# Kernel tuning notes

Measured on AMD Instinct MI355X. Metric: run time of the kernel, lower is better.

## Reference

```python
import jax, jax.numpy as jnp
import numpy as np

D_MODEL = 1024
N_HEADS = 16
DEPTH = D_MODEL // N_HEADS
B, S = 2, 2048


def layer_norm(x, gamma, beta):
    # Faithful to the torch module: unbiased std (ddof=1), eps added to std.
    mean = jnp.mean(x, axis=-1, keepdims=True)
    std = jnp.std(x, axis=-1, ddof=1, keepdims=True)
    return gamma * ((x - mean) / (std + 1e-6)) + beta


def setup_inputs() -> dict:
    key = jax.random.key(0)
    ks = jax.random.split(key, 12)
    sc = 0.02
    x = jax.random.normal(ks[0], (B, S, D_MODEL), jnp.float32)
    mask = jnp.triu(jnp.ones((S, S), jnp.float32), k=1)  # 1 where masked (future)
    return {
        "x": x,
        "mask": mask,
        "wq_w": jax.random.normal(ks[1], (D_MODEL, D_MODEL), jnp.float32) * sc,
        "wq_b": jnp.zeros((D_MODEL,), jnp.float32),
        "wk_w": jax.random.normal(ks[2], (D_MODEL, D_MODEL), jnp.float32) * sc,
        "wk_b": jnp.zeros((D_MODEL,), jnp.float32),
        "wv_w": jax.random.normal(ks[3], (D_MODEL, D_MODEL), jnp.float32) * sc,
        "wv_b": jnp.zeros((D_MODEL,), jnp.float32),
        "dense_w": jax.random.normal(ks[4], (D_MODEL, D_MODEL), jnp.float32) * sc,
        "dense_b": jnp.zeros((D_MODEL,), jnp.float32),
        "gamma1": jnp.ones((D_MODEL,), jnp.float32),
        "beta1": jnp.zeros((D_MODEL,), jnp.float32),
        "gamma2": jnp.ones((D_MODEL,), jnp.float32),
        "beta2": jnp.zeros((D_MODEL,), jnp.float32),
        "fc_w": jax.random.normal(ks[5], (4 * D_MODEL, D_MODEL), jnp.float32) * sc,
        "proj_w": jax.random.normal(ks[6], (D_MODEL, 4 * D_MODEL), jnp.float32) * sc,
    }


def reference(x, mask, wq_w, wq_b, wk_w, wk_b, wv_w, wv_b, dense_w, dense_b,
              gamma1, beta1, gamma2, beta2, fc_w, proj_w):
    # x: [B,S,D]. Dropout is identity in eval.
    xn = layer_norm(x, gamma1, beta1)

    def split(h):  # [B,S,D] -> [B,H,S,depth]
        return h.reshape(B, S, N_HEADS, DEPTH).transpose(0, 2, 1, 3)

    q = split(xn @ wq_w.T + wq_b)
    k = split(xn @ wk_w.T + wk_b)
    v = split(xn @ wv_w.T + wv_b)

    scores = jnp.einsum("bhqd,bhkd->bhqk", q, k) / jnp.sqrt(
        jnp.asarray(DEPTH, jnp.float32))
    scores = scores + mask * -1e9
    attn = jax.nn.softmax(scores, axis=-1)
    ctx = jnp.einsum("bhqk,bhkd->bhqd", attn, v)
    ctx = ctx.transpose(0, 2, 1, 3).reshape(B, S, D_MODEL)
    attn_out = ctx @ dense_w.T + dense_b

    # Residual adds the *normed* x (faithful to the original ordering).
    h = xn + attn_out
    hn = layer_norm(h, gamma2, beta2)

    ff = jax.nn.gelu(hn @ fc_w.T, approximate=False) @ proj_w.T
    return hn + ff
```

## Files before the change

kernel.cpp:

```cpp
#include <hip/hip_runtime.h>
#include <math.h>

typedef __bf16 bf16;
typedef __attribute__((ext_vector_type(2))) __bf16 bf16x2;
typedef __attribute__((ext_vector_type(4))) __bf16 bf16x4;
typedef __attribute__((ext_vector_type(8))) __bf16 bf16x8;
typedef __attribute__((ext_vector_type(4))) float f32x4;

#define D_MODEL 1024
#define NH 16
#define DP 64
#define BB 2
#define SEQ 2048
#define TOK 4096
#define FFD 4096
#define AST 72

__device__ __forceinline__ void async16(bf16* lds, const bf16* g) {
    __builtin_amdgcn_global_load_lds(
        (__attribute__((address_space(1))) void*)g,
        (__attribute__((address_space(3))) void*)lds, 16, 0, 0);
}

__device__ __forceinline__ f32x4 mfma16(bf16x8 a, bf16x8 b, f32x4 c) {
    return __builtin_amdgcn_mfma_f32_16x16x32_bf16(a, b, c, 0, 0, 0);
}

struct CvtArgs {
    const float4* in[6];
    bf16x4* out[6];
};
__global__ __launch_bounds__(256) void cvt_all(CvtArgs a)
{
    const int i = blockIdx.x * 256 + threadIdx.x;
    int seg, idx;
    if (i < (1 << 20)) { seg = i >> 18; idx = i & ((1 << 18) - 1); }
    else {
        const int j = i - (1 << 20);
        seg = 4 + (j >> 20); idx = j & ((1 << 20) - 1);
    }
    const float4 v = a.in[seg][idx];
    bf16x4 o; o[0] = (bf16)v.x; o[1] = (bf16)v.y; o[2] = (bf16)v.z; o[3] = (bf16)v.w;
    a.out[seg][idx] = o;
}

template<typename TIN>
__global__ __launch_bounds__(256) void ln_kernel(
    const TIN* __restrict__ in, const float* __restrict__ g,
    const float* __restrict__ be, bf16* __restrict__ out)
{
    const size_t row = blockIdx.x;
    const int t = threadIdx.x;
    const TIN* x = in + row * D_MODEL;

    float v0, v1, v2, v3;
    if constexpr (sizeof(TIN) == 4) {
        const float4 xv = *(const float4*)(x + t * 4);
        v0 = xv.x; v1 = xv.y; v2 = xv.z; v3 = xv.w;
    } else {
        const bf16x4 xv = *(const bf16x4*)(x + t * 4);
        v0 = (float)xv[0]; v1 = (float)xv[1]; v2 = (float)xv[2]; v3 = (float)xv[3];
    }
    float s  = v0 + v1 + v2 + v3;
    float ss = v0*v0 + v1*v1 + v2*v2 + v3*v3;
    #pragma unroll
    for (int off = 32; off > 0; off >>= 1) {
        s  += __shfl_down(s, off);
        ss += __shfl_down(ss, off);
    }
    __shared__ float rs[4], rss[4];
    if ((t & 63) == 0) { rs[t >> 6] = s; rss[t >> 6] = ss; }
    __syncthreads();
    const float S  = rs[0] + rs[1] + rs[2] + rs[3];
    const float SS = rss[0] + rss[1] + rss[2] + rss[3];
    const float mean = S * (1.0f / 1024.0f);
    const float var  = fmaxf((SS - S * mean) * (1.0f / 1023.0f), 0.0f);
    const float inv  = 1.0f / (sqrtf(var) + 1e-6f);

    const float4 gv = *(const float4*)(g  + t * 4);
    const float4 bv = *(const float4*)(be + t * 4);
    bf16x4 ov;
    ov[0] = (bf16)(gv.x * ((v0 - mean) * inv) + bv.x);
    ov[1] = (bf16)(gv.y * ((v1 - mean) * inv) + bv.y);
    ov[2] = (bf16)(gv.z * ((v2 - mean) * inv) + bv.z);
    ov[3] = (bf16)(gv.w * ((v3 - mean) * inv) + bv.w);
    *(bf16x4*)(out + row * D_MODEL + t * 4) = ov;
}

template<int EPI, typename TOUT>
__global__ __launch_bounds__(256, 2) void gemm_bt(
    const bf16* __restrict__ A, const bf16* __restrict__ W,
    const float* __restrict__ bias, const bf16* res,
    TOUT* C, int M, int N, int K, float scale)
{
    __shared__ __align__(16) bf16 As[128 * 32];
    __shared__ __align__(16) bf16 Bs[128 * 32];
    const int t = threadIdx.x;
    const int w = t >> 6, lane = t & 63;
    const int fr = lane & 15, quad = lane >> 4;
    const int m0 = blockIdx.y * 128, n0 = blockIdx.x * 128;
    const int wm = (w >> 1) * 64, wn = (w & 1) * 64;

    const f32x4 z = {0.f, 0.f, 0.f, 0.f};
    f32x4 acc[4][4];
    #pragma unroll
    for (int i = 0; i < 4; ++i)
        #pragma unroll
        for (int j = 0; j < 4; ++j) acc[i][j] = z;

    const int nk = K >> 5;
    for (int kt = 0; kt < nk; ++kt) {
        const int k0 = kt << 5;
        #pragma unroll
        for (int call = 0; call < 2; ++call) {
            const int c = call * 256 + t;
            const int row = c >> 2, sub = c & 3;
            async16(&As[(size_t)(call * 256 + w * 64) * 8],
                    A + (size_t)(m0 + row) * K + k0 + sub * 8);
            async16(&Bs[(size_t)(call * 256 + w * 64) * 8],
                    W + (size_t)(n0 + row) * K + k0 + sub * 8);
        }
        __syncthreads();
        bf16x8 af[4], bfr[4];
        #pragma unroll
        for (int i = 0; i < 4; ++i)
            af[i] = *(const bf16x8*)&As[(wm + i * 16 + fr) * 32 + quad * 8];
        #pragma unroll
        for (int j = 0; j < 4; ++j)
            bfr[j] = *(const bf16x8*)&Bs[(wn + j * 16 + fr) * 32 + quad * 8];
        #pragma unroll
        for (int i = 0; i < 4; ++i)
            #pragma unroll
            for (int j = 0; j < 4; ++j)
                acc[i][j] = mfma16(af[i], bfr[j], acc[i][j]);
        __syncthreads();
    }

    #pragma unroll
    for (int i = 0; i < 4; ++i) {
        #pragma unroll
        for (int j = 0; j < 4; ++j) {
            #pragma unroll
            for (int r = 0; r < 4; ++r) {
                const int m = m0 + wm + i * 16 + quad * 4 + r;
                const int n = n0 + wn + j * 16 + fr;
                float v = acc[i][j][r];
                if (EPI == 1) {
                    v += bias[n];
                    v += (float)res[(size_t)m * N + n];
                    C[(size_t)m * N + n] = (TOUT)v;
                } else if (EPI == 2) {
                    v = 0.5f * v * (1.0f + erff(v * 0.70710678118f));
                    C[(size_t)m * N + n] = (TOUT)v;
                } else {
                    v += (float)res[(size_t)m * N + n];
                    C[(size_t)m * N + n] = (TOUT)v;
                }
            }
        }
    }
}

template<int EPI, typename TOUT>
__global__ __launch_bounds__(256, 2) void gemm_bt64(
    const bf16* __restrict__ A, const bf16* __restrict__ W,
    const float* __restrict__ bias, const bf16* res,
    TOUT* C, int M, int N, int K)
{
    __shared__ __align__(16) bf16 As[128 * 32];
    __shared__ __align__(16) bf16 Bs[64 * 32];
    const int t = threadIdx.x;
    const int w = t >> 6, lane = t & 63;
    const int fr = lane & 15, quad = lane >> 4;
    const int m0 = blockIdx.y * 128, n0 = blockIdx.x * 64;
    const int wm = (w >> 1) * 64, wn = (w & 1) * 32;

    const f32x4 z = {0.f, 0.f, 0.f, 0.f};
    f32x4 acc[4][2];
    #pragma unroll
    for (int i = 0; i < 4; ++i)
        #pragma unroll
        for (int j = 0; j < 2; ++j) acc[i][j] = z;

    const int nk = K >> 5;
    for (int kt = 0; kt < nk; ++kt) {
        const int k0 = kt << 5;
        #pragma unroll
        for (int call = 0; call < 2; ++call) {
            const int c = call * 256 + t;
            const int row = c >> 2, sub = c & 3;
            async16(&As[(size_t)(call * 256 + w * 64) * 8],
                    A + (size_t)(m0 + row) * K + k0 + sub * 8);
        }
        {
            const int row = t >> 2, sub = t & 3;
            async16(&Bs[(size_t)(w * 64) * 8],
                    W + (size_t)(n0 + row) * K + k0 + sub * 8);
        }
        __syncthreads();
        bf16x8 af[4], bfr[2];
        #pragma unroll
        for (int i = 0; i < 4; ++i)
            af[i] = *(const bf16x8*)&As[(wm + i * 16 + fr) * 32 + quad * 8];
        #pragma unroll
        for (int j = 0; j < 2; ++j)
            bfr[j] = *(const bf16x8*)&Bs[(wn + j * 16 + fr) * 32 + quad * 8];
        #pragma unroll
        for (int i = 0; i < 4; ++i)
            #pragma unroll
            for (int j = 0; j < 2; ++j)
                acc[i][j] = mfma16(af[i], bfr[j], acc[i][j]);
        __syncthreads();
    }

    #pragma unroll
    for (int i = 0; i < 4; ++i) {
        #pragma unroll
        for (int j = 0; j < 2; ++j) {
            #pragma unroll
            for (int r = 0; r < 4; ++r) {
                const int m = m0 + wm + i * 16 + quad * 4 + r;
                const int n = n0 + wn + j * 16 + fr;
                float v = acc[i][j][r];
                if (EPI == 1) {
                    v += bias[n];
                    v += (float)res[(size_t)m * N + n];
                    C[(size_t)m * N + n] = (TOUT)v;
                } else {
                    v += (float)res[(size_t)m * N + n];
                    C[(size_t)m * N + n] = (TOUT)v;
                }
            }
        }
    }
}

__global__ __launch_bounds__(256, 2) void gemm_qkv(
    const bf16* __restrict__ A,
    const bf16* __restrict__ wq, const bf16* __restrict__ wk,
    const bf16* __restrict__ wvv,
    const float* __restrict__ bq, const float* __restrict__ bk,
    const float* __restrict__ bv,
    bf16* __restrict__ outq, bf16* __restrict__ outk, bf16* __restrict__ outv)
{
    const int sel = blockIdx.x >> 3;
    const bf16* W = (sel == 0) ? wq : ((sel == 1) ? wk : wvv);
    const float* bias = (sel == 0) ? bq : ((sel == 1) ? bk : bv);
    bf16* C = (sel == 0) ? outq : ((sel == 1) ? outk : outv);
    const float scale = (sel == 0) ? 0.125f : 1.0f;
    const int K = D_MODEL;

    __shared__ __align__(16) bf16 As[128 * 32];
    __shared__ __align__(16) bf16 Bs[128 * 32];
    const int t = threadIdx.x;
    const int w = t >> 6, lane = t & 63;
    const int fr = lane & 15, quad = lane >> 4;
    const int m0 = blockIdx.y * 128, n0 = (blockIdx.x & 7) * 128;
    const int wm = (w >> 1) * 64, wn = (w & 1) * 64;

    const f32x4 z = {0.f, 0.f, 0.f, 0.f};
    f32x4 acc[4][4];
    #pragma unroll
    for (int i = 0; i < 4; ++i)
        #pragma unroll
        for (int j = 0; j < 4; ++j) acc[i][j] = z;

    for (int kt = 0; kt < (D_MODEL >> 5); ++kt) {
        const int k0 = kt << 5;
        #pragma unroll
        for (int call = 0; call < 2; ++call) {
            const int c = call * 256 + t;
            const int row = c >> 2, sub = c & 3;
            async16(&As[(size_t)(call * 256 + w * 64) * 8],
                    A + (size_t)(m0 + row) * K + k0 + sub * 8);
            async16(&Bs[(size_t)(call * 256 + w * 64) * 8],
                    W + (size_t)(n0 + row) * K + k0 + sub * 8);
        }
        __syncthreads();
        bf16x8 af[4], bfr[4];
        #pragma unroll
        for (int i = 0; i < 4; ++i)
            af[i] = *(const bf16x8*)&As[(wm + i * 16 + fr) * 32 + quad * 8];
        #pragma unroll
        for (int j = 0; j < 4; ++j)
            bfr[j] = *(const bf16x8*)&Bs[(wn + j * 16 + fr) * 32 + quad * 8];
        #pragma unroll
        for (int i = 0; i < 4; ++i)
            #pragma unroll
            for (int j = 0; j < 4; ++j)
                acc[i][j] = mfma16(af[i], bfr[j], acc[i][j]);
        __syncthreads();
    }

    #pragma unroll
    for (int i = 0; i < 4; ++i)
        #pragma unroll
        for (int j = 0; j < 4; ++j)
            #pragma unroll
            for (int r = 0; r < 4; ++r) {
                const int m = m0 + wm + i * 16 + quad * 4 + r;
                const int n = n0 + wn + j * 16 + fr;
                const float vv = (acc[i][j][r] + bias[n]) * scale;
                const int b = m >> 11, s = m & 2047, h = n >> 6, d = n & 63;
                C[(((size_t)(b * NH + h)) * SEQ + s) * DP + d] = (bf16)vv;
            }
}

__global__ __launch_bounds__(256, 2) void attn_kernel(
    const bf16* __restrict__ q, const bf16* __restrict__ k,
    const bf16* __restrict__ v, bf16* __restrict__ ctx)
{
    __shared__ __align__(16) bf16 Ks[2][64 * AST];
    __shared__ __align__(16) bf16 VsT[2][64 * AST];
    __shared__ __align__(16) bf16 Ps[4][16 * AST];
    const int t = threadIdx.x, wv = t >> 6, lane = t & 63;
    const int fr = lane & 15, quad = lane >> 4;
    const int bh = blockIdx.y;
    const size_t base = (size_t)bh * SEQ * DP;
    const int b = bh >> 4, hh = bh & 15;
    const f32x4 z = {0.f, 0.f, 0.f, 0.f};
    const int krow = t >> 2, kd0 = (t & 3) * 16;
    const int pp = t & 31, c0 = (t >> 5) * 8;

    for (int half = 0; half < 2; ++half) {
        const int qt = half ? (31 - (int)blockIdx.x) : (int)blockIdx.x;
        const int q0 = qt * 64, qr0 = q0 + wv * 16;
        const int nkt = qt + 1;

        __syncthreads();

        bf16x8 qf[2];
        #pragma unroll
        for (int c = 0; c < 2; ++c)
            qf[c] = *(const bf16x8*)(q + base + (size_t)(qr0 + fr) * DP + c * 32 + quad * 8);

        bf16x8 k0r, k1r, v0r, v1r;
        {
            const bf16* kp = k + base + (size_t)krow * DP + kd0;
            k0r = *(const bf16x8*)kp; k1r = *(const bf16x8*)(kp + 8);
            const bf16* vp = v + base + (size_t)(2 * pp) * DP + c0;
            v0r = *(const bf16x8*)vp; v1r = *(const bf16x8*)(vp + DP);
        }

        f32x4 o[4] = {z, z, z, z};
        float mi[4] = {-1e30f, -1e30f, -1e30f, -1e30f};
        float li[4] = {0.f, 0.f, 0.f, 0.f};

        for (int kt = 0; kt < nkt; ++kt) {
            const int cur = kt & 1;
            const int kk0 = kt * 64;
            *(bf16x8*)&Ks[cur][krow * AST + kd0]     = k0r;
            *(bf16x8*)&Ks[cur][krow * AST + kd0 + 8] = k1r;
            #pragma unroll
            for (int j = 0; j < 8; ++j) {
                bf16x2 pr; pr[0] = v0r[j]; pr[1] = v1r[j];
                *(bf16x2*)&VsT[cur][(c0 + j) * AST + 2 * pp] = pr;
            }
            __syncthreads();
            if (kt + 1 < nkt) {
                const bf16* kp = k + base + (size_t)(kk0 + 64 + krow) * DP + kd0;
                k0r = *(const bf16x8*)kp; k1r = *(const bf16x8*)(kp + 8);
                const bf16* vp = v + base + (size_t)(kk0 + 64 + 2 * pp) * DP + c0;
                v0r = *(const bf16x8*)vp; v1r = *(const bf16x8*)(vp + DP);
            }

            f32x4 sa[4] = {z, z, z, z};
            #pragma unroll
            for (int nb = 0; nb < 4; ++nb)
                #pragma unroll
                for (int c = 0; c < 2; ++c) {
                    const bf16x8 kf = *(const bf16x8*)&Ks[cur][(nb * 16 + fr) * AST + c * 32 + quad * 8];
                    sa[nb] = mfma16(qf[c], kf, sa[nb]);
                }

            float p[4][4], rmax[4];
            #pragma unroll
            for (int r = 0; r < 4; ++r) rmax[r] = -1e30f;
            #pragma unroll
            for (int nb = 0; nb < 4; ++nb)
                #pragma unroll
                for (int r = 0; r < 4; ++r) {
                    const int key = kk0 + nb * 16 + fr;
                    const int qrow = qr0 + quad * 4 + r;
                    float sv = sa[nb][r];
                    if (key > qrow) sv += -1e9f;
                    p[nb][r] = sv;
                    rmax[r] = fmaxf(rmax[r], sv);
                }
            #pragma unroll
            for (int off = 1; off < 16; off <<= 1)
                #pragma unroll
                for (int r = 0; r < 4; ++r)
                    rmax[r] = fmaxf(rmax[r], __shfl_xor(rmax[r], off));

            float alpha[4], psum[4];
            #pragma unroll
            for (int r = 0; r < 4; ++r) {
                const float nm = fmaxf(mi[r], rmax[r]);
                alpha[r] = __expf(mi[r] - nm);
                mi[r] = nm;
                float ps = 0.f;
                #pragma unroll
                for (int nb = 0; nb < 4; ++nb) {
                    const float e = __expf(p[nb][r] - nm);
                    p[nb][r] = e;
                    ps += e;
                }
                psum[r] = ps;
            }
            #pragma unroll
            for (int off = 1; off < 16; off <<= 1)
                #pragma unroll
                for (int r = 0; r < 4; ++r)
                    psum[r] += __shfl_xor(psum[r], off);
            #pragma unroll
            for (int r = 0; r < 4; ++r) li[r] = li[r] * alpha[r] + psum[r];
            #pragma unroll
            for (int db = 0; db < 4; ++db)
                #pragma unroll
                for (int r = 0; r < 4; ++r) o[db][r] *= alpha[r];

            #pragma unroll
            for (int nb = 0; nb < 4; ++nb)
                #pragma unroll
                for (int r = 0; r < 4; ++r)
                    Ps[wv][(quad * 4 + r) * AST + nb * 16 + fr] = (bf16)p[nb][r];

            bf16x8 pf[2];
            #pragma unroll
            for (int c = 0; c < 2; ++c)
                pf[c] = *(const bf16x8*)&Ps[wv][fr * AST + c * 32 + quad * 8];
            #pragma unroll
            for (int db = 0; db < 4; ++db)
                #pragma unroll
                for (int c = 0; c < 2; ++c) {
                    const bf16x8 vf = *(const bf16x8*)&VsT[cur][(db * 16 + fr) * AST + c * 32 + quad * 8];
                    o[db] = mfma16(pf[c], vf, o[db]);
                }
        }

        #pragma unroll
        for (int db = 0; db < 4; ++db)
            #pragma unroll
            for (int r = 0; r < 4; ++r) {
                const int qrow = qr0 + quad * 4 + r;
                const int d = db * 16 + fr;
                ctx[((size_t)(b * SEQ + qrow)) * D_MODEL + hh * DP + d] =
                    (bf16)(o[db][r] / li[r]);
            }
    }
}

extern "C" void kernel_launch(void* const* d_in, const int* in_sizes, int n_in,
                              void* d_out, int out_size, void* d_ws, size_t ws_size,
                              hipStream_t stream) {
    const float* x       = (const float*)d_in[0];
    const float* wq_w    = (const float*)d_in[2];
    const float* wq_b    = (const float*)d_in[3];
    const float* wk_w    = (const float*)d_in[4];
    const float* wk_b    = (const float*)d_in[5];
    const float* wv_w    = (const float*)d_in[6];
    const float* wv_b    = (const float*)d_in[7];
    const float* dense_w = (const float*)d_in[8];
    const float* dense_b = (const float*)d_in[9];
    const float* gamma1  = (const float*)d_in[10];
    const float* beta1   = (const float*)d_in[11];
    const float* gamma2  = (const float*)d_in[12];
    const float* beta2   = (const float*)d_in[13];
    const float* fc_w    = (const float*)d_in[14];
    const float* proj_w  = (const float*)d_in[15];
    float* out = (float*)d_out;

    bf16* ws = (bf16*)d_ws;
    const size_t M1 = (size_t)1 << 20;
    bf16* xn   = ws;
    bf16* qb   = ws + 4 * M1;
    bf16* kb   = ws + 8 * M1;
    bf16* vb   = ws + 12 * M1;
    bf16* ctx  = ws + 16 * M1;
    bf16* ff1  = qb;
    bf16* wqc  = ws + 20 * M1;
    bf16* wkc  = ws + 21 * M1;
    bf16* wvc  = ws + 22 * M1;
    bf16* wdc  = ws + 23 * M1;
    bf16* fcc  = ws + 24 * M1;
    bf16* prjc = ws + 28 * M1;
    bf16* h = xn, *hn = xn;

    CvtArgs ca;
    ca.in[0] = (const float4*)wq_w;    ca.out[0] = (bf16x4*)wqc;
    ca.in[1] = (const float4*)wk_w;    ca.out[1] = (bf16x4*)wkc;
    ca.in[2] = (const float4*)wv_w;    ca.out[2] = (bf16x4*)wvc;
    ca.in[3] = (const float4*)dense_w; ca.out[3] = (bf16x4*)wdc;
    ca.in[4] = (const float4*)fc_w;    ca.out[4] = (bf16x4*)fcc;
    ca.in[5] = (const float4*)proj_w;  ca.out[5] = (bf16x4*)prjc;
    cvt_all<<<12288, 256, 0, stream>>>(ca);

    ln_kernel<float><<<TOK, 256, 0, stream>>>(x, gamma1, beta1, xn);
    gemm_qkv<<<dim3(24, 32), 256, 0, stream>>>(xn, wqc, wkc, wvc,
                                               wq_b, wk_b, wv_b, qb, kb, vb);
    attn_kernel<<<dim3(16, BB * NH), 256, 0, stream>>>(qb, kb, vb, ctx);
    gemm_bt64<1, bf16><<<dim3(16, 32), 256, 0, stream>>>(ctx, wdc, dense_b, xn, h,
                                                         TOK, D_MODEL, D_MODEL);
    ln_kernel<bf16><<<TOK, 256, 0, stream>>>(h, gamma2, beta2, hn);
    gemm_bt<2, bf16><<<dim3(32, 32), 256, 0, stream>>>(hn, fcc, nullptr, nullptr, ff1,
                                                       TOK, FFD, D_MODEL, 1.0f);
    gemm_bt64<3, float><<<dim3(16, 32), 256, 0, stream>>>(ff1, prjc, nullptr, hn, out,
                                                          TOK, D_MODEL, FFD);
}
```

Measured before the change: 404.6 us.

## Double-buffer LDS tiles in GEMM kernels to prefetch next K-slice

The three GEMM kernels (gemm_bt, gemm_bt64, gemm_qkv) now use two LDS buffers for each operand. The first K-tile is loaded before the loop, and each iteration issues async loads for the next tile while running MFMAs on the current one. This hides global-to-LDS load latency behind compute and drops one barrier per iteration. In exchange, LDS use per block doubles, and overlap only happens if the end-of-loop barrier's memory wait falls after the MFMAs.

```diff
diff --git a/kernel.cpp b/kernel.cpp
--- a/kernel.cpp
+++ b/kernel.cpp
@@ -93,8 +93,8 @@
     const float* __restrict__ bias, const bf16* res,
     TOUT* C, int M, int N, int K, float scale)
 {
-    __shared__ __align__(16) bf16 As[128 * 32];
-    __shared__ __align__(16) bf16 Bs[128 * 32];
+    __shared__ __align__(16) bf16 As[2][128 * 32];
+    __shared__ __align__(16) bf16 Bs[2][128 * 32];
     const int t = threadIdx.x;
     const int w = t >> 6, lane = t & 63;
     const int fr = lane & 15, quad = lane >> 4;
@@ -109,25 +109,38 @@
         for (int j = 0; j < 4; ++j) acc[i][j] = z;
 
     const int nk = K >> 5;
+    const int srow = t >> 2, ssub = t & 3;
+
+    #pragma unroll
+    for (int call = 0; call < 2; ++call) {
+        const int row = call * 64 + srow;
+        async16(&As[0][(size_t)(call * 256 + w * 64) * 8],
+                A + (size_t)(m0 + row) * K + ssub * 8);
+        async16(&Bs[0][(size_t)(call * 256 + w * 64) * 8],
+                W + (size_t)(n0 + row) * K + ssub * 8);
+    }
+    __syncthreads();
+
     for (int kt = 0; kt < nk; ++kt) {
-        const int k0 = kt << 5;
-        #pragma unroll
-        for (int call = 0; call < 2; ++call) {
-            const int c = call * 256 + t;
-            const int row = c >> 2, sub = c & 3;
-            async16(&As[(size_t)(call * 256 + w * 64) * 8],
-                    A + (size_t)(m0 + row) * K + k0 + sub * 8);
-            async16(&Bs[(size_t)(call * 256 + w * 64) * 8],
-                    W + (size_t)(n0 + row) * K + k0 + sub * 8);
-        }
-        __syncthreads();
+        const int cur = kt & 1;
+        if (kt + 1 < nk) {
+            const int k0 = (kt + 1) << 5;
+            #pragma unroll
+            for (int call = 0; call < 2; ++call) {
+                const int row = call * 64 + srow;
+                async16(&As[cur ^ 1][(size_t)(call * 256 + w * 64) * 8],
+                        A + (size_t)(m0 + row) * K + k0 + ssub * 8);
+                async16(&Bs[cur ^ 1][(size_t)(call * 256 + w * 64) * 8],
+                        W + (size_t)(n0 + row) * K + k0 + ssub * 8);
+            }
+        }
         bf16x8 af[4], bfr[4];
         #pragma unroll
         for (int i = 0; i < 4; ++i)
-            af[i] = *(const bf16x8*)&As[(wm + i * 16 + fr) * 32 + quad * 8];
+            af[i] = *(const bf16x8*)&As[cur][(wm + i * 16 + fr) * 32 + quad * 8];
         #pragma unroll
         for (int j = 0; j < 4; ++j)
-            bfr[j] = *(const bf16x8*)&Bs[(wn + j * 16 + fr) * 32 + quad * 8];
+            bfr[j] = *(const bf16x8*)&Bs[cur][(wn + j * 16 + fr) * 32 + quad * 8];
         #pragma unroll
         for (int i = 0; i < 4; ++i)
             #pragma unroll
@@ -167,8 +180,8 @@
     const float* __restrict__ bias, const bf16* res,
     TOUT* C, int M, int N, int K)
 {
-    __shared__ __align__(16) bf16 As[128 * 32];
-    __shared__ __align__(16) bf16 Bs[64 * 32];
+    __shared__ __align__(16) bf16 As[2][128 * 32];
+    __shared__ __align__(16) bf16 Bs[2][64 * 32];
     const int t = threadIdx.x;
     const int w = t >> 6, lane = t & 63;
     const int fr = lane & 15, quad = lane >> 4;
@@ -183,28 +196,38 @@
         for (int j = 0; j < 2; ++j) acc[i][j] = z;
 
     const int nk = K >> 5;
+    const int srow = t >> 2, ssub = t & 3;
+
+    #pragma unroll
+    for (int call = 0; call < 2; ++call) {
+        const int row = call * 64 + srow;
+        async16(&As[0][(size_t)(call * 256 + w * 64) * 8],
+                A + (size_t)(m0 + row) * K + ssub * 8);
+    }
+    async16(&Bs[0][(size_t)(w * 64) * 8],
+            W + (size_t)(n0 + srow) * K + ssub * 8);
+    __syncthreads();
+
     for (int kt = 0; kt < nk; ++kt) {
-        const int k0 = kt << 5;
-        #pragma unroll
-        for (int call = 0; call < 2; ++call) {
-            const int c = call * 256 + t;
-            const int row = c >> 2, sub = c & 3;
-            async16(&As[(size_t)(call * 256 + w * 64) * 8],
-                    A + (size_t)(m0 + row) * K + k0 + sub * 8);
-        }
-        {
-            const int row = t >> 2, sub = t & 3;
-            async16(&Bs[(size_t)(w * 64) * 8],
-                    W + (size_t)(n0 + row) * K + k0 + sub * 8);
-        }
-        __syncthreads();
+        const int cur = kt & 1;
+        if (kt + 1 < nk) {
+            const int k0 = (kt + 1) << 5;
+            #pragma unroll
+            for (int call = 0; call < 2; ++call) {
+                const int row = call * 64 + srow;
+                async16(&As[cur ^ 1][(size_t)(call * 256 + w * 64) * 8],
+                        A + (size_t)(m0 + row) * K + k0 + ssub * 8);
+            }
+            async16(&Bs[cur ^ 1][(size_t)(w * 64) * 8],
+                    W + (size_t)(n0 + srow) * K + k0 + ssub * 8);
+        }
         bf16x8 af[4], bfr[2];
         #pragma unroll
         for (int i = 0; i < 4; ++i)
-            af[i] = *(const bf16x8*)&As[(wm + i * 16 + fr) * 32 + quad * 8];
+            af[i] = *(const bf16x8*)&As[cur][(wm + i * 16 + fr) * 32 + quad * 8];
         #pragma unroll
         for (int j = 0; j < 2; ++j)
-            bfr[j] = *(const bf16x8*)&Bs[(wn + j * 16 + fr) * 32 + quad * 8];
+            bfr[j] = *(const bf16x8*)&Bs[cur][(wn + j * 16 + fr) * 32 + quad * 8];
         #pragma unroll
         for (int i = 0; i < 4; ++i)
             #pragma unroll
@@ -250,8 +273,8 @@
     const float scale = (sel == 0) ? 0.125f : 1.0f;
     const int K = D_MODEL;
 
-    __shared__ __align__(16) bf16 As[128 * 32];
-    __shared__ __align__(16) bf16 Bs[128 * 32];
+    __shared__ __align__(16) bf16 As[2][128 * 32];
+    __shared__ __align__(16) bf16 Bs[2][128 * 32];
     const int t = threadIdx.x;
     const int w = t >> 6, lane = t & 63;
     const int fr = lane & 15, quad = lane >> 4;
@@ -265,25 +288,39 @@
         #pragma unroll
         for (int j = 0; j < 4; ++j) acc[i][j] = z;
 
-    for (int kt = 0; kt < (D_MODEL >> 5); ++kt) {
-        const int k0 = kt << 5;
-        #pragma unroll
-        for (int call = 0; call < 2; ++call) {
-            const int c = call * 256 + t;
-            const int row = c >> 2, sub = c & 3;
-            async16(&As[(size_t)(call * 256 + w * 64) * 8],
-                    A + (size_t)(m0 + row) * K + k0 + sub * 8);
-            async16(&Bs[(size_t)(call * 256 + w * 64) * 8],
-                    W + (size_t)(n0 + row) * K + k0 + sub * 8);
-        }
-        __syncthreads();
+    const int nk = D_MODEL >> 5;
+    const int srow = t >> 2, ssub = t & 3;
+
+    #pragma unroll
+    for (int call = 0; call < 2; ++call) {
+        const int row = call * 64 + srow;
+        async16(&As[0][(size_t)(call * 256 + w * 64) * 8],
+                A + (size_t)(m0 + row) * K + ssub * 8);
+        async16(&Bs[0][(size_t)(call * 256 + w * 64) * 8],
+                W + (size_t)(n0 + row) * K + ssub * 8);
+    }
+    __syncthreads();
+
+    for (int kt = 0; kt < nk; ++kt) {
+        const int cur = kt & 1;
+        if (kt + 1 < nk) {
+            const int k0 = (kt + 1) << 5;
+            #pragma unroll
+            for (int call = 0; call < 2; ++call) {
+                const int row = call * 64 + srow;
+                async16(&As[cur ^ 1][(size_t)(call * 256 + w * 64) * 8],
+                        A + (size_t)(m0 + row) * K + k0 + ssub * 8);
+                async16(&Bs[cur ^ 1][(size_t)(call * 256 + w * 64) * 8],
+                        W + (size_t)(n0 + row) * K + k0 + ssub * 8);
+            }
+        }
         bf16x8 af[4], bfr[4];
         #pragma unroll
         for (int i = 0; i < 4; ++i)
-            af[i] = *(const bf16x8*)&As[(wm + i * 16 + fr) * 32 + quad * 8];
+            af[i] = *(const bf16x8*)&As[cur][(wm + i * 16 + fr) * 32 + quad * 8];
         #pragma unroll
         for (int j = 0; j < 4; ++j)
-            bfr[j] = *(const bf16x8*)&Bs[(wn + j * 16 + fr) * 32 + quad * 8];
+            bfr[j] = *(const bf16x8*)&Bs[cur][(wn + j * 16 + fr) * 32 + quad * 8];
         #pragma unroll
         for (int i = 0; i < 4; ++i)
             #pragma unroll
```

New measurement: 388.8 us. 1.04x faster.

## Pipeline GEMM K-loop with 4-stage async LDS buffers, XOR swizzle, and attention tweaks

Applied to the files above, without the earlier changes.

The three GEMM kernels move from single-buffered LDS loads, with two __syncthreads per K step, to a 4-deep ring of async global-to-LDS buffers. Each step waits with explicit vmcnt counts and a single barrier, prefetching three tiles ahead. The LDS tile columns are XOR-swizzled to cut bank conflicts on the MFMA fragment reads. The attention kernel remaps block IDs so neighbouring blocks spread across heads, and raises wave priority around its MFMA sections. The costs are 4x the LDS use per block, which can lower occupancy, and hand-tuned waitcnt counts that are fragile if the number of loads changes.

```diff
diff --git a/kernel.cpp b/kernel.cpp
--- a/kernel.cpp
+++ b/kernel.cpp
@@ -87,14 +87,15 @@
     *(bf16x4*)(out + row * D_MODEL + t * 4) = ov;
 }
 
+
 template<int EPI, typename TOUT>
 __global__ __launch_bounds__(256, 2) void gemm_bt(
     const bf16* __restrict__ A, const bf16* __restrict__ W,
     const float* __restrict__ bias, const bf16* res,
     TOUT* C, int M, int N, int K, float scale)
 {
-    __shared__ __align__(16) bf16 As[128 * 32];
-    __shared__ __align__(16) bf16 Bs[128 * 32];
+    __shared__ __align__(16) bf16 As[4][128 * 32];
+    __shared__ __align__(16) bf16 Bs[4][128 * 32];
     const int t = threadIdx.x;
     const int w = t >> 6, lane = t & 63;
     const int fr = lane & 15, quad = lane >> 4;
@@ -109,32 +110,52 @@
         for (int j = 0; j < 4; ++j) acc[i][j] = z;
 
     const int nk = K >> 5;
+    const int srow = t >> 2;
+    const int ssub = (t & 3) ^ (srow & 3);
+    const int xs = fr & 3;
+
+    #define STAGE_BT(kt, b) {                                                  \
+        const int k0_ = (kt) << 5;                                             \
+        _Pragma("unroll")                                                      \
+        for (int call = 0; call < 2; ++call) {                                 \
+            const int row = call * 64 + srow;                                  \
+            async16(&As[b][(size_t)(call * 256 + w * 64) * 8],                 \
+                    A + (size_t)(m0 + row) * K + k0_ + ssub * 8);              \
+            async16(&Bs[b][(size_t)(call * 256 + w * 64) * 8],                 \
+                    W + (size_t)(n0 + row) * K + k0_ + ssub * 8);              \
+        }                                                                      \
+    }
+
+    STAGE_BT(0, 0); STAGE_BT(1, 1); STAGE_BT(2, 2);
+
     for (int kt = 0; kt < nk; ++kt) {
-        const int k0 = kt << 5;
-        #pragma unroll
-        for (int call = 0; call < 2; ++call) {
-            const int c = call * 256 + t;
-            const int row = c >> 2, sub = c & 3;
-            async16(&As[(size_t)(call * 256 + w * 64) * 8],
-                    A + (size_t)(m0 + row) * K + k0 + sub * 8);
-            async16(&Bs[(size_t)(call * 256 + w * 64) * 8],
-                    W + (size_t)(n0 + row) * K + k0 + sub * 8);
-        }
-        __syncthreads();
+        const int cur = kt & 3;
+        if (kt + 2 < nk)      asm volatile("s_waitcnt vmcnt(8)" ::: "memory");
+        else if (kt + 1 < nk) asm volatile("s_waitcnt vmcnt(4)" ::: "memory");
+        else                  asm volatile("s_waitcnt vmcnt(0)" ::: "memory");
+        __builtin_amdgcn_sched_barrier(0);
+        __builtin_amdgcn_s_barrier();
+        asm volatile("" ::: "memory");
+
+        if (kt + 3 < nk) STAGE_BT(kt + 3, (kt + 3) & 3);
+
         bf16x8 af[4], bfr[4];
         #pragma unroll
         for (int i = 0; i < 4; ++i)
-            af[i] = *(const bf16x8*)&As[(wm + i * 16 + fr) * 32 + quad * 8];
+            af[i] = *(const bf16x8*)&As[cur][(wm + i * 16 + fr) * 32 + (quad ^ xs) * 8];
         #pragma unroll
         for (int j = 0; j < 4; ++j)
-            bfr[j] = *(const bf16x8*)&Bs[(wn + j * 16 + fr) * 32 + quad * 8];
+            bfr[j] = *(const bf16x8*)&Bs[cur][(wn + j * 16 + fr) * 32 + (quad ^ xs) * 8];
         #pragma unroll
         for (int i = 0; i < 4; ++i)
             #pragma unroll
             for (int j = 0; j < 4; ++j)
                 acc[i][j] = mfma16(af[i], bfr[j], acc[i][j]);
-        __syncthreads();
-    }
+
+        asm volatile("s_waitcnt lgkmcnt(0)" ::: "memory");
+        __builtin_amdgcn_sched_barrier(0);
+    }
+    #undef STAGE_BT
 
     #pragma unroll
     for (int i = 0; i < 4; ++i) {
@@ -167,8 +188,8 @@
     const float* __restrict__ bias, const bf16* res,
     TOUT* C, int M, int N, int K)
 {
-    __shared__ __align__(16) bf16 As[128 * 32];
-    __shared__ __align__(16) bf16 Bs[64 * 32];
+    __shared__ __align__(16) bf16 As[4][128 * 32];
+    __shared__ __align__(16) bf16 Bs[4][64 * 32];
     const int t = threadIdx.x;
     const int w = t >> 6, lane = t & 63;
     const int fr = lane & 15, quad = lane >> 4;
@@ -183,35 +204,52 @@
         for (int j = 0; j < 2; ++j) acc[i][j] = z;
 
     const int nk = K >> 5;
+    const int srow = t >> 2;
+    const int ssub = (t & 3) ^ (srow & 3);
+    const int xs = fr & 3;
+
+    #define STAGE_BT64(kt, b) {                                                \
+        const int k0_ = (kt) << 5;                                             \
+        _Pragma("unroll")                                                      \
+        for (int call = 0; call < 2; ++call) {                                 \
+            const int row = call * 64 + srow;                                  \
+            async16(&As[b][(size_t)(call * 256 + w * 64) * 8],                 \
+                    A + (size_t)(m0 + row) * K + k0_ + ssub * 8);              \
+        }                                                                      \
+        async16(&Bs[b][(size_t)(w * 64) * 8],                                  \
+                W + (size_t)(n0 + srow) * K + k0_ + ssub * 8);                 \
+    }
+
+    STAGE_BT64(0, 0); STAGE_BT64(1, 1); STAGE_BT64(2, 2);
+
     for (int kt = 0; kt < nk; ++kt) {
-        const int k0 = kt << 5;
-        #pragma unroll
-        for (int call = 0; call < 2; ++call) {
-            const int c = call * 256 + t;
-            const int row = c >> 2, sub = c & 3;
-            async16(&As[(size_t)(call * 256 + w * 64) * 8],
-                    A + (size_t)(m0 + row) * K + k0 + sub * 8);
-        }
-        {
-            const int row = t >> 2, sub = t & 3;
-            async16(&Bs[(size_t)(w * 64) * 8],
-                    W + (size_t)(n0 + row) * K + k0 + sub * 8);
-        }
-        __syncthreads();
+        const int cur = kt & 3;
+        if (kt + 2 < nk)      asm volatile("s_waitcnt vmcnt(6)" ::: "memory");
+        else if (kt + 1 < nk) asm volatile("s_waitcnt vmcnt(3)" ::: "memory");
+        else                  asm volatile("s_waitcnt vmcnt(0)" ::: "memory");
+        __builtin_amdgcn_sched_barrier(0);
+        __builtin_amdgcn_s_barrier();
+        asm volatile("" ::: "memory");
+
+        if (kt + 3 < nk) STAGE_BT64(kt + 3, (kt + 3) & 3);
+
         bf16x8 af[4], bfr[2];
         #pragma unroll
         for (int i = 0; i < 4; ++i)
-            af[i] = *(const bf16x8*)&As[(wm + i * 16 + fr) * 32 + quad * 8];
+            af[i] = *(const bf16x8*)&As[cur][(wm + i * 16 + fr) * 32 + (quad ^ xs) * 8];
         #pragma unroll
         for (int j = 0; j < 2; ++j)
-            bfr[j] = *(const bf16x8*)&Bs[(wn + j * 16 + fr) * 32 + quad * 8];
+            bfr[j] = *(const bf16x8*)&Bs[cur][(wn + j * 16 + fr) * 32 + (quad ^ xs) * 8];
         #pragma unroll
         for (int i = 0; i < 4; ++i)
             #pragma unroll
             for (int j = 0; j < 2; ++j)
                 acc[i][j] = mfma16(af[i], bfr[j], acc[i][j]);
-        __syncthreads();
-    }
+
+        asm volatile("s_waitcnt lgkmcnt(0)" ::: "memory");
+        __builtin_amdgcn_sched_barrier(0);
+    }
+    #undef STAGE_BT64
 
     #pragma unroll
     for (int i = 0; i < 4; ++i) {
@@ -250,8 +288,8 @@
     const float scale = (sel == 0) ? 0.125f : 1.0f;
     const int K = D_MODEL;
 
-    __shared__ __align__(16) bf16 As[128 * 32];
-    __shared__ __align__(16) bf16 Bs[128 * 32];
+    __shared__ __align__(16) bf16 As[4][128 * 32];
+    __shared__ __align__(16) bf16 Bs[4][128 * 32];
     const int t = threadIdx.x;
     const int w = t >> 6, lane = t & 63;
     const int fr = lane & 15, quad = lane >> 4;
@@ -265,32 +303,53 @@
         #pragma unroll
         for (int j = 0; j < 4; ++j) acc[i][j] = z;
 
-    for (int kt = 0; kt < (D_MODEL >> 5); ++kt) {
-        const int k0 = kt << 5;
-        #pragma unroll
-        for (int call = 0; call < 2; ++call) {
-            const int c = call * 256 + t;
-            const int row = c >> 2, sub = c & 3;
-            async16(&As[(size_t)(call * 256 + w * 64) * 8],
-                    A + (size_t)(m0 + row) * K + k0 + sub * 8);
-            async16(&Bs[(size_t)(call * 256 + w * 64) * 8],
-                    W + (size_t)(n0 + row) * K + k0 + sub * 8);
-        }
-        __syncthreads();
+    const int nk = D_MODEL >> 5;
+    const int srow = t >> 2;
+    const int ssub = (t & 3) ^ (srow & 3);
+    const int xs = fr & 3;
+
+    #define STAGE_QKV(kt, b) {                                                 \
+        const int k0_ = (kt) << 5;                                             \
+        _Pragma("unroll")                                                      \
+        for (int call = 0; call < 2; ++call) {                                 \
+            const int row = call * 64 + srow;                                  \
+            async16(&As[b][(size_t)(call * 256 + w * 64) * 8],                 \
+                    A + (size_t)(m0 + row) * K + k0_ + ssub * 8);              \
+            async16(&Bs[b][(size_t)(call * 256 + w * 64) * 8],                 \
+                    W + (size_t)(n0 + row) * K + k0_ + ssub * 8);              \
+        }                                                                      \
+    }
+
+    STAGE_QKV(0, 0); STAGE_QKV(1, 1); STAGE_QKV(2, 2);
+
+    for (int kt = 0; kt < nk; ++kt) {
+        const int cur = kt & 3;
+        if (kt + 2 < nk)      asm volatile("s_waitcnt vmcnt(8)" ::: "memory");
+        else if (kt + 1 < nk) asm volatile("s_waitcnt vmcnt(4)" ::: "memory");
+        else                  asm volatile("s_waitcnt vmcnt(0)" ::: "memory");
+        __builtin_amdgcn_sched_barrier(0);
+        __builtin_amdgcn_s_barrier();
+        asm volatile("" ::: "memory");
+
+        if (kt + 3 < nk) STAGE_QKV(kt + 3, (kt + 3) & 3);
+
         bf16x8 af[4], bfr[4];
         #pragma unroll
         for (int i = 0; i < 4; ++i)
-            af[i] = *(const bf16x8*)&As[(wm + i * 16 + fr) * 32 + quad * 8];
+            af[i] = *(const bf16x8*)&As[cur][(wm + i * 16 + fr) * 32 + (quad ^ xs) * 8];
         #pragma unroll
         for (int j = 0; j < 4; ++j)
-            bfr[j] = *(const bf16x8*)&Bs[(wn + j * 16 + fr) * 32 + quad * 8];
+            bfr[j] = *(const bf16x8*)&Bs[cur][(wn + j * 16 + fr) * 32 + (quad ^ xs) * 8];
         #pragma unroll
         for (int i = 0; i < 4; ++i)
             #pragma unroll
             for (int j = 0; j < 4; ++j)
                 acc[i][j] = mfma16(af[i], bfr[j], acc[i][j]);
-        __syncthreads();
-    }
+
+        asm volatile("s_waitcnt lgkmcnt(0)" ::: "memory");
+        __builtin_amdgcn_sched_barrier(0);
+    }
+    #undef STAGE_QKV
 
     #pragma unroll
     for (int i = 0; i < 4; ++i)
@@ -315,7 +374,10 @@
     __shared__ __align__(16) bf16 Ps[4][16 * AST];
     const int t = threadIdx.x, wv = t >> 6, lane = t & 63;
     const int fr = lane & 15, quad = lane >> 4;
-    const int bh = blockIdx.y;
+    const int id = blockIdx.y * 16 + blockIdx.x;
+    const int nid = (id & 7) * 64 + (id >> 3);
+    const int bh = nid >> 4;
+    const int qxi = nid & 15;
     const size_t base = (size_t)bh * SEQ * DP;
     const int b = bh >> 4, hh = bh & 15;
     const f32x4 z = {0.f, 0.f, 0.f, 0.f};
@@ -323,7 +385,7 @@
     const int pp = t & 31, c0 = (t >> 5) * 8;
 
     for (int half = 0; half < 2; ++half) {
-        const int qt = half ? (31 - (int)blockIdx.x) : (int)blockIdx.x;
+        const int qt = half ? (31 - qxi) : qxi;
         const int q0 = qt * 64, qr0 = q0 + wv * 16;
         const int nkt = qt + 1;
 
@@ -365,6 +427,7 @@
             }
 
             f32x4 sa[4] = {z, z, z, z};
+            __builtin_amdgcn_s_setprio(1);
             #pragma unroll
             for (int nb = 0; nb < 4; ++nb)
                 #pragma unroll
@@ -372,6 +435,7 @@
                     const bf16x8 kf = *(const bf16x8*)&Ks[cur][(nb * 16 + fr) * AST + c * 32 + quad * 8];
                     sa[nb] = mfma16(qf[c], kf, sa[nb]);
                 }
+            __builtin_amdgcn_s_setprio(0);
 
             float p[4][4], rmax[4];
             #pragma unroll
@@ -430,6 +494,7 @@
             #pragma unroll
             for (int c = 0; c < 2; ++c)
                 pf[c] = *(const bf16x8*)&Ps[wv][fr * AST + c * 32 + quad * 8];
+            __builtin_amdgcn_s_setprio(1);
             #pragma unroll
             for (int db = 0; db < 4; ++db)
                 #pragma unroll
@@ -437,6 +502,7 @@
                     const bf16x8 vf = *(const bf16x8*)&VsT[cur][(db * 16 + fr) * AST + c * 32 + quad * 8];
                     o[db] = mfma16(pf[c], vf, o[db]);
                 }
+            __builtin_amdgcn_s_setprio(0);
         }
 
         #pragma unroll
```

Result: slower. 430.6 us (+6.4%).
